# Kernel optimization log

Measured on AMD Instinct MI355X. Metric: run time of the kernel, lower is better.

## Reference

```python
import jax, jax.numpy as jnp
import numpy as np

B, H, S, D = 2, 16, 2048, 64


def setup_inputs() -> dict:
    key = jax.random.key(0)
    kq, kk, kv = jax.random.split(key, 3)
    queries = jax.random.normal(kq, (B, H, S, D), dtype=jnp.float32)
    keys = jax.random.normal(kk, (B, H, S, D), dtype=jnp.float32)
    values = jax.random.normal(kv, (B, H, S, D), dtype=jnp.float32)
    scaling_factor = jnp.asarray(np.sqrt(D), dtype=jnp.float32)
    # causal mask, broadcast over heads: True = attend
    causal = jnp.tril(jnp.ones((S, S), dtype=bool))
    mask = jnp.broadcast_to(causal[None, None, :, :], (B, 1, S, S))
    return {
        "queries": queries,
        "keys": keys,
        "values": values,
        "scaling_factor": scaling_factor,
        "mask": mask,
    }


def reference(queries, keys, values, scaling_factor, mask):
    # scores: [B, H, S, S]
    scores = jnp.einsum("bhqd,bhkd->bhqk", queries, keys) / scaling_factor
    scores = jnp.where(mask, scores, -jnp.inf)
    attn = jax.nn.softmax(scores, axis=-1)
    # embeddings: [B, H, S, D]
    return jnp.einsum("bhqk,bhkd->bhqd", attn, values)
```

## Files before the change

kernel.cpp:

```cpp
#include <hip/hip_runtime.h>
#include <hip/hip_bf16.h>


typedef __attribute__((ext_vector_type(8))) short bf16x8;
typedef __attribute__((ext_vector_type(4))) float f32x4;
typedef unsigned uint2v __attribute__((ext_vector_type(2)));

#define MFMA32K(a, b, c) __builtin_amdgcn_mfma_f32_16x16x32_bf16(a, b, c, 0, 0, 0)

constexpr int Bsz = 2, Hn = 16, Sn = 2048, Dn = 64;
constexpr int KBLK = 64;
constexpr int NE = Bsz * Hn * Sn * Dn;

#if defined(__has_builtin)
#if __has_builtin(__builtin_amdgcn_exp2f)
#define EXP2(x) __builtin_amdgcn_exp2f(x)
#endif
#endif
#ifndef EXP2
#define EXP2(x) exp2f(x)
#endif

__device__ inline short f2bf(float f) {
  union { float f; unsigned u; } v;
  v.f = f;
  unsigned r = v.u + 0x7FFF + ((v.u >> 16) & 1);
  return (short)(r >> 16);
}

__device__ inline unsigned pk_bf16(float lo, float hi) {
  unsigned r;
  asm("v_cvt_pk_bf16_f32 %0, %1, %2" : "=v"(r) : "v"(lo), "v"(hi));
  return r;
}

__device__ inline void gl2lds16(const void* g, void* l) {
  __builtin_amdgcn_global_load_lds(
      (const __attribute__((address_space(1))) unsigned int*)g,
      (__attribute__((address_space(3))) unsigned int*)l, 16, 0, 0);
}

__device__ inline int swz(int row, int colbyte) {
  return row * 128 + (colbyte ^ ((row & 7) << 4));
}

#if defined(__has_builtin)
#if __has_builtin(__builtin_amdgcn_permlane16_swap) && \
    __has_builtin(__builtin_amdgcn_permlane32_swap)
#define HAVE_PERMLANE_SWAP 1
#endif
#endif

__device__ inline float xred_max(float x) {
#ifdef HAVE_PERMLANE_SWAP
  uint2v a = __builtin_amdgcn_permlane16_swap(__float_as_uint(x),
                                              __float_as_uint(x), false, false);
  x = fmaxf(__uint_as_float(a[0]), __uint_as_float(a[1]));
  uint2v b = __builtin_amdgcn_permlane32_swap(__float_as_uint(x),
                                              __float_as_uint(x), false, false);
  x = fmaxf(__uint_as_float(b[0]), __uint_as_float(b[1]));
#else
  x = fmaxf(x, __shfl_xor(x, 16, 64));
  x = fmaxf(x, __shfl_xor(x, 32, 64));
#endif
  return x;
}

__global__ __launch_bounds__(256) void prep(const float* __restrict__ K,
                                            const float* __restrict__ V,
                                            short* __restrict__ Kb,
                                            short* __restrict__ Vt) {
  __shared__ short t[64][66];
  const int tile = blockIdx.x, bh = blockIdx.y;
  const int tid = threadIdx.x;
  const int r = tid >> 2, c = (tid & 3) * 16;
  const size_t base = (size_t)bh * Sn * Dn;

  {
    const float* kp = K + base + (size_t)(tile * 64 + r) * Dn + c;
    float4 x0 = *(const float4*)(kp + 0);
    float4 x1 = *(const float4*)(kp + 4);
    float4 x2 = *(const float4*)(kp + 8);
    float4 x3 = *(const float4*)(kp + 12);
    bf16x8 w0, w1;
    w0[0] = f2bf(x0.x); w0[1] = f2bf(x0.y); w0[2] = f2bf(x0.z); w0[3] = f2bf(x0.w);
    w0[4] = f2bf(x1.x); w0[5] = f2bf(x1.y); w0[6] = f2bf(x1.z); w0[7] = f2bf(x1.w);
    w1[0] = f2bf(x2.x); w1[1] = f2bf(x2.y); w1[2] = f2bf(x2.z); w1[3] = f2bf(x2.w);
    w1[4] = f2bf(x3.x); w1[5] = f2bf(x3.y); w1[6] = f2bf(x3.z); w1[7] = f2bf(x3.w);
    short* op = Kb + base + (size_t)(tile * 64 + r) * Dn + c;
    *(bf16x8*)op = w0;
    *(bf16x8*)(op + 8) = w1;
  }
  {
    const float* vp = V + base + (size_t)(tile * 64 + r) * Dn + c;
    float4 x0 = *(const float4*)(vp + 0);
    float4 x1 = *(const float4*)(vp + 4);
    float4 x2 = *(const float4*)(vp + 8);
    float4 x3 = *(const float4*)(vp + 12);
    short* tr = &t[r][c];
    tr[0] = f2bf(x0.x); tr[1] = f2bf(x0.y); tr[2] = f2bf(x0.z); tr[3] = f2bf(x0.w);
    tr[4] = f2bf(x1.x); tr[5] = f2bf(x1.y); tr[6] = f2bf(x1.z); tr[7] = f2bf(x1.w);
    tr[8] = f2bf(x2.x); tr[9] = f2bf(x2.y); tr[10] = f2bf(x2.z); tr[11] = f2bf(x2.w);
    tr[12] = f2bf(x3.x); tr[13] = f2bf(x3.y); tr[14] = f2bf(x3.z); tr[15] = f2bf(x3.w);
    __syncthreads();
    short* op = Vt + base + (size_t)r * Sn + tile * 64 + c;
    bf16x8 w0, w1;
#pragma unroll
    for (int j = 0; j < 8; ++j) {
      int p0 = c + j, p1 = c + 8 + j;
      int k0 = 32 * (p0 >> 5) + 16 * ((p0 >> 2) & 1) + 4 * ((p0 >> 3) & 3) + (p0 & 3);
      int k1 = 32 * (p1 >> 5) + 16 * ((p1 >> 2) & 1) + 4 * ((p1 >> 3) & 3) + (p1 & 3);
      w0[j] = t[k0][r];
      w1[j] = t[k1][r];
    }
    *(bf16x8*)op = w0;
    *(bf16x8*)(op + 8) = w1;
  }
}

__global__ __launch_bounds__(256, 4) void attn_fwd(
    const float* __restrict__ Q, const short* __restrict__ Kb,
    const short* __restrict__ Vt, const float* __restrict__ SF,
    float* __restrict__ O) {
  __shared__ short Kbuf[2][64 * 64];
  __shared__ short Vbuf[2][64 * 64];

  const int bh = blockIdx.x;
  const int qt = (gridDim.y - 1) - blockIdx.y;
  const int tid = threadIdx.x;
  const int wave = tid >> 6, lane = tid & 63;
  const int qh = wave >> 1, par = wave & 1;
  const int g = lane >> 4, lc = lane & 15;
  const float qscale = 1.4426950408889634f / SF[0];

  const size_t base = (size_t)bh * Sn * Dn;
  const char* Kg = (const char*)(Kb + base);
  const char* Vg = (const char*)(Vt + base);
  const int nkv = qt + 1;
  const int npairs = (nkv + 1) >> 1;

  int qg[2];
  qg[0] = qt * 64 + qh * 32 + lc;
  qg[1] = qg[0] + 16;

  int ka[4][2], va[2][4];
#pragma unroll
  for (int t = 0; t < 4; ++t) {
    ka[t][0] = swz(t * 16 + lc, g * 16);
    ka[t][1] = swz(t * 16 + lc, g * 16 + 64);
  }
#pragma unroll
  for (int t2 = 0; t2 < 2; ++t2)
#pragma unroll
    for (int dt = 0; dt < 4; ++dt)
      va[t2][dt] = swz(dt * 16 + lc, t2 * 64 + g * 16);
  int koff[2], voff[2];
#pragma unroll
  for (int j = 0; j < 2; ++j) {
    int off = (wave * 2 + j) * 1024 + lane * 16;
    int row = off >> 7;
    int col = (off & 127) ^ ((row & 7) << 4);
    koff[j] = row * 128 + col;
    voff[j] = row * 4096 + col;
  }

  auto stageK = [&](int kt, int buf) {
    const char* src = Kg + (size_t)kt * 8192;
#pragma unroll
    for (int j = 0; j < 2; ++j)
      gl2lds16(src + koff[j], (char*)Kbuf[buf] + (wave * 2 + j) * 1024);
  };
  auto stageV = [&](int kt, int buf) {
    const char* src = Vg + (size_t)kt * 128;
#pragma unroll
    for (int j = 0; j < 2; ++j)
      gl2lds16(src + voff[j], (char*)Vbuf[buf] + (wave * 2 + j) * 1024);
  };

  bf16x8 bq[2][2];
#pragma unroll
  for (int u = 0; u < 2; ++u) {
    const float* qp = Q + base + (size_t)qg[u] * Dn + g * 8;
#pragma unroll
    for (int h = 0; h < 2; ++h) {
      float4 x0 = *(const float4*)(qp + 32 * h);
      float4 x1 = *(const float4*)(qp + 32 * h + 4);
      bf16x8 a;
      a[0] = f2bf(x0.x * qscale); a[1] = f2bf(x0.y * qscale);
      a[2] = f2bf(x0.z * qscale); a[3] = f2bf(x0.w * qscale);
      a[4] = f2bf(x1.x * qscale); a[5] = f2bf(x1.y * qscale);
      a[6] = f2bf(x1.z * qscale); a[7] = f2bf(x1.w * qscale);
      bq[u][h] = a;
    }
  }

  bf16x8 ones;
#pragma unroll
  for (int j = 0; j < 8; ++j) ones[j] = (short)0x3F80;

  f32x4 o[2][4], lsum[2];
  float m[2] = {-10000.0f, -10000.0f};
#pragma unroll
  for (int u = 0; u < 2; ++u) {
    lsum[u] = (f32x4){0.f, 0.f, 0.f, 0.f};
#pragma unroll
    for (int dt = 0; dt < 4; ++dt) o[u][dt] = (f32x4){0.f, 0.f, 0.f, 0.f};
  }

  stageK(0, 0);
  stageV(0, 0);
  if (nkv > 1) { stageK(1, 1); stageV(1, 1); }
  __syncthreads();

  for (int j = 0; j < npairs; ++j) {
    const int myt = 2 * j + par;
    if (myt < nkv) {
      const char* Kc = (const char*)Kbuf[par];
      const char* Vc = (const char*)Vbuf[par];

      f32x4 s[2][4];
      __builtin_amdgcn_s_setprio(1);
#pragma unroll
      for (int t = 0; t < 4; ++t) {
        bf16x8 ak0 = *(const bf16x8*)(Kc + ka[t][0]);
        bf16x8 ak1 = *(const bf16x8*)(Kc + ka[t][1]);
#pragma unroll
        for (int u = 0; u < 2; ++u) {
          f32x4 z = (f32x4){0.f, 0.f, 0.f, 0.f};
          z = MFMA32K(ak0, bq[u][0], z);
          z = MFMA32K(ak1, bq[u][1], z);
          s[u][t] = z;
        }
      }
      __builtin_amdgcn_s_setprio(0);

      if (myt == qt) {
        const int kb = myt * KBLK;
#pragma unroll
        for (int u = 0; u < 2; ++u)
#pragma unroll
          for (int t = 0; t < 4; ++t)
#pragma unroll
            for (int i = 0; i < 4; ++i) {
              int kg = kb + t * 16 + g * 4 + i;
              if (kg > qg[u]) s[u][t][i] = -30000.0f;
            }
      }

      union { unsigned uu[4]; bf16x8 v; } pb[2][2];
#pragma unroll
      for (int u = 0; u < 2; ++u) {
        float a0 = fmaxf(fmaxf(s[u][0][0], s[u][0][1]), s[u][0][2]);
        float a1 = fmaxf(fmaxf(s[u][0][3], s[u][1][0]), s[u][1][1]);
        float a2 = fmaxf(fmaxf(s[u][1][2], s[u][1][3]), s[u][2][0]);
        float a3 = fmaxf(fmaxf(s[u][2][1], s[u][2][2]), s[u][2][3]);
        float a4 = fmaxf(fmaxf(s[u][3][0], s[u][3][1]), s[u][3][2]);
        float b0 = fmaxf(fmaxf(a0, a1), a2);
        float b1 = fmaxf(fmaxf(a3, a4), s[u][3][3]);
        float plocal = fmaxf(b0, b1);
        if (!__all(plocal - m[u] <= 8.0f)) {
          float pmax = xred_max(plocal);
          float mnew = fmaxf(m[u], pmax);
          float alpha = EXP2(m[u] - mnew);
          lsum[u][0] *= alpha;
#pragma unroll
          for (int dt = 0; dt < 4; ++dt) o[u][dt] *= alpha;
          m[u] = mnew;
        }
#pragma unroll
        for (int t = 0; t < 4; ++t)
#pragma unroll
          for (int i = 0; i < 4; ++i) s[u][t][i] = EXP2(s[u][t][i] - m[u]);
#pragma unroll
        for (int t2 = 0; t2 < 2; ++t2) {
          pb[u][t2].uu[0] = pk_bf16(s[u][2 * t2][0], s[u][2 * t2][1]);
          pb[u][t2].uu[1] = pk_bf16(s[u][2 * t2][2], s[u][2 * t2][3]);
          pb[u][t2].uu[2] = pk_bf16(s[u][2 * t2 + 1][0], s[u][2 * t2 + 1][1]);
          pb[u][t2].uu[3] = pk_bf16(s[u][2 * t2 + 1][2], s[u][2 * t2 + 1][3]);
        }
      }

      __builtin_amdgcn_s_setprio(1);
#pragma unroll
      for (int t2 = 0; t2 < 2; ++t2) {
        lsum[0] = MFMA32K(ones, pb[0][t2].v, lsum[0]);
        lsum[1] = MFMA32K(ones, pb[1][t2].v, lsum[1]);
#pragma unroll
        for (int dt = 0; dt < 4; ++dt) {
          bf16x8 av = *(const bf16x8*)(Vc + va[t2][dt]);
          o[0][dt] = MFMA32K(av, pb[0][t2].v, o[0][dt]);
          o[1][dt] = MFMA32K(av, pb[1][t2].v, o[1][dt]);
        }
      }
      __builtin_amdgcn_s_setprio(0);
    }

    __syncthreads();

    const int nt0 = 2 * j + 2;
    if (nt0 < nkv) { stageK(nt0, 0); stageV(nt0, 0); }
    if (nt0 + 1 < nkv) { stageK(nt0 + 1, 1); stageV(nt0 + 1, 1); }
    __syncthreads();
  }

  float* scr = (qh == 0) ? (float*)&Kbuf[0][0] : (float*)&Vbuf[0][0];
  if (par == 1) {
#pragma unroll
    for (int u = 0; u < 2; ++u) {
#pragma unroll
      for (int dt = 0; dt < 4; ++dt)
        *(f32x4*)(scr + (u * 16 + lc) * 64 + dt * 16 + g * 4) = o[u][dt];
      if (g == 0) {
        scr[2048 + u * 16 + lc] = m[u];
        scr[2080 + u * 16 + lc] = lsum[u][0];
      }
    }
  }
  __syncthreads();
  if (par == 0) {
#pragma unroll
    for (int u = 0; u < 2; ++u) {
      float mB = scr[2048 + u * 16 + lc];
      float lB = scr[2080 + u * 16 + lc];
      float M = fmaxf(m[u], mB);
      float aA = EXP2(m[u] - M), aB = EXP2(mB - M);
      float inv = 1.0f / (lsum[u][0] * aA + lB * aB);
      float cA = aA * inv, cB = aB * inv;
      float* op = O + base + (size_t)qg[u] * Dn;
#pragma unroll
      for (int dt = 0; dt < 4; ++dt) {
        f32x4 oB = *(const f32x4*)(scr + (u * 16 + lc) * 64 + dt * 16 + g * 4);
        f32x4 r = o[u][dt] * cA + oB * cB;
        *(f32x4*)(op + dt * 16 + g * 4) = r;
      }
    }
  }
}

extern "C" void kernel_launch(void* const* d_in, const int* in_sizes, int n_in,
                              void* d_out, int out_size, void* d_ws, size_t ws_size,
                              hipStream_t stream) {
  const float* Q = (const float*)d_in[0];
  const float* K = (const float*)d_in[1];
  const float* V = (const float*)d_in[2];
  const float* SF = (const float*)d_in[3];
  float* O = (float*)d_out;

  short* Kb = (short*)d_ws;
  short* Vt = Kb + NE;

  prep<<<dim3(Sn / 64, Bsz * Hn), 256, 0, stream>>>(K, V, Kb, Vt);
  attn_fwd<<<dim3(Bsz * Hn, Sn / 64), 256, 0, stream>>>(Q, Kb, Vt, SF, O);
}
```

Before: 44.39 us.

## Split long causal query tiles across two KV chunks with a combine kernel

Query tiles 16-31, the ones with the longest causal KV ranges, are now each split into two blocks covering KV tiles 0-15 and 16-qt. Each block writes an unnormalized partial output plus its max and sum to workspace, and a new combine kernel merges them with log-sum-exp rescaling. The aim is to shorten the critical path of the heaviest blocks and balance the load across the grid (48 y-blocks instead of 32). In exchange it adds an extra kernel launch, partial-output traffic through global memory, and extra workspace that must fit in the provided buffer.

```diff
diff --git a/kernel.cpp b/kernel.cpp
--- a/kernel.cpp
+++ b/kernel.cpp
@@ -11,6 +11,7 @@
 constexpr int Bsz = 2, Hn = 16, Sn = 2048, Dn = 64;
 constexpr int KBLK = 64;
 constexpr int NE = Bsz * Hn * Sn * Dn;
+constexpr int NPART = Bsz * Hn * 16 * 2;
 
 #if defined(__has_builtin)
 #if __has_builtin(__builtin_amdgcn_exp2f)
@@ -121,12 +122,18 @@
 __global__ __launch_bounds__(256, 4) void attn_fwd(
     const float* __restrict__ Q, const short* __restrict__ Kb,
     const short* __restrict__ Vt, const float* __restrict__ SF,
-    float* __restrict__ O) {
+    float* __restrict__ O, float* __restrict__ Opart,
+    float* __restrict__ MLpart) {
   __shared__ short Kbuf[2][64 * 64];
   __shared__ short Vbuf[2][64 * 64];
 
   const int bh = blockIdx.x;
-  const int qt = (gridDim.y - 1) - blockIdx.y;
+  const int qy = blockIdx.y;
+  const int qt = (qy < 16) ? (31 - qy) : (47 - qy);
+  const int chunk = (qy >= 16 && qy < 32) ? 1 : 0;
+  const int t0 = chunk * 16;
+  const int t1 = (qy < 16) ? 15 : qt;
+
   const int tid = threadIdx.x;
   const int wave = tid >> 6, lane = tid & 63;
   const int qh = wave >> 1, par = wave & 1;
@@ -136,8 +143,6 @@
   const size_t base = (size_t)bh * Sn * Dn;
   const char* Kg = (const char*)(Kb + base);
   const char* Vg = (const char*)(Vt + base);
-  const int nkv = qt + 1;
-  const int npairs = (nkv + 1) >> 1;
 
   int qg[2];
   qg[0] = qt * 64 + qh * 32 + lc;
@@ -207,14 +212,15 @@
     for (int dt = 0; dt < 4; ++dt) o[u][dt] = (f32x4){0.f, 0.f, 0.f, 0.f};
   }
 
-  stageK(0, 0);
-  stageV(0, 0);
-  if (nkv > 1) { stageK(1, 1); stageV(1, 1); }
+  stageK(t0, 0);
+  stageV(t0, 0);
+  if (t0 + 1 <= t1) { stageK(t0 + 1, 1); stageV(t0 + 1, 1); }
   __syncthreads();
 
+  const int npairs = ((t1 - t0 + 1) + 1) >> 1;
   for (int j = 0; j < npairs; ++j) {
-    const int myt = 2 * j + par;
-    if (myt < nkv) {
+    const int myt = t0 + 2 * j + par;
+    if (myt <= t1) {
       const char* Kc = (const char*)Kbuf[par];
       const char* Vc = (const char*)Vbuf[par];
 
@@ -297,9 +303,9 @@
 
     __syncthreads();
 
-    const int nt0 = 2 * j + 2;
-    if (nt0 < nkv) { stageK(nt0, 0); stageV(nt0, 0); }
-    if (nt0 + 1 < nkv) { stageK(nt0 + 1, 1); stageV(nt0 + 1, 1); }
+    const int nt0 = t0 + 2 * j + 2;
+    if (nt0 <= t1) { stageK(nt0, 0); stageV(nt0, 0); }
+    if (nt0 + 1 <= t1) { stageK(nt0 + 1, 1); stageV(nt0 + 1, 1); }
     __syncthreads();
   }
 
@@ -324,16 +330,61 @@
       float lB = scr[2080 + u * 16 + lc];
       float M = fmaxf(m[u], mB);
       float aA = EXP2(m[u] - M), aB = EXP2(mB - M);
-      float inv = 1.0f / (lsum[u][0] * aA + lB * aB);
-      float cA = aA * inv, cB = aB * inv;
-      float* op = O + base + (size_t)qg[u] * Dn;
-#pragma unroll
-      for (int dt = 0; dt < 4; ++dt) {
-        f32x4 oB = *(const f32x4*)(scr + (u * 16 + lc) * 64 + dt * 16 + g * 4);
-        f32x4 r = o[u][dt] * cA + oB * cB;
-        *(f32x4*)(op + dt * 16 + g * 4) = r;
+      float lC = lsum[u][0] * aA + lB * aB;
+      if (qy >= 32) {
+        float inv = 1.0f / lC;
+        float cA = aA * inv, cB = aB * inv;
+        float* op = O + base + (size_t)qg[u] * Dn;
+#pragma unroll
+        for (int dt = 0; dt < 4; ++dt) {
+          f32x4 oB = *(const f32x4*)(scr + (u * 16 + lc) * 64 + dt * 16 + g * 4);
+          f32x4 r = o[u][dt] * cA + oB * cB;
+          *(f32x4*)(op + dt * 16 + g * 4) = r;
+        }
+      } else {
+        const int p = (bh * 16 + (qt - 16)) * 2 + chunk;
+        const int row = qh * 32 + u * 16 + lc;
+        float* op = Opart + (size_t)p * 4096 + row * 64;
+#pragma unroll
+        for (int dt = 0; dt < 4; ++dt) {
+          f32x4 oB = *(const f32x4*)(scr + (u * 16 + lc) * 64 + dt * 16 + g * 4);
+          f32x4 r = o[u][dt] * aA + oB * aB;
+          *(f32x4*)(op + dt * 16 + g * 4) = r;
+        }
+        if (g == 0) ((float2*)MLpart)[p * 64 + row] = make_float2(M, lC);
       }
     }
+  }
+}
+
+__global__ __launch_bounds__(256) void combine(const float* __restrict__ Opart,
+                                               const float* __restrict__ MLpart,
+                                               float* __restrict__ O) {
+  const int bx = blockIdx.x;
+  const int bh = bx >> 4, qh = bx & 15, qt = 16 + qh;
+  const int p0 = (bh * 16 + qh) * 2;
+  const int tid = threadIdx.x;
+  const int r = tid >> 2, dc = (tid & 3) * 16;
+
+  const float2 ml0 = ((const float2*)MLpart)[p0 * 64 + r];
+  const float2 ml1 = ((const float2*)MLpart)[(p0 + 1) * 64 + r];
+  const float M = fmaxf(ml0.x, ml1.x);
+  const float s0 = EXP2(ml0.x - M), s1 = EXP2(ml1.x - M);
+  const float inv = 1.0f / (ml0.y * s0 + ml1.y * s1);
+
+  const float* a = Opart + (size_t)p0 * 4096 + r * 64 + dc;
+  const float* b = a + 4096;
+  float* op = O + (size_t)bh * Sn * Dn + (size_t)(qt * 64 + r) * Dn + dc;
+#pragma unroll
+  for (int j = 0; j < 4; ++j) {
+    float4 x = *(const float4*)(a + j * 4);
+    float4 y = *(const float4*)(b + j * 4);
+    float4 z;
+    z.x = (x.x * s0 + y.x * s1) * inv;
+    z.y = (x.y * s0 + y.y * s1) * inv;
+    z.z = (x.z * s0 + y.z * s1) * inv;
+    z.w = (x.w * s0 + y.w * s1) * inv;
+    *(float4*)(op + j * 4) = z;
   }
 }
 
@@ -348,7 +399,11 @@
 
   short* Kb = (short*)d_ws;
   short* Vt = Kb + NE;
+  float* Opart = (float*)(Vt + NE);
+  float* MLpart = Opart + (size_t)NPART * 4096;
 
   prep<<<dim3(Sn / 64, Bsz * Hn), 256, 0, stream>>>(K, V, Kb, Vt);
-  attn_fwd<<<dim3(Bsz * Hn, Sn / 64), 256, 0, stream>>>(Q, Kb, Vt, SF, O);
-}
+  attn_fwd<<<dim3(Bsz * Hn, 48), 256, 0, stream>>>(Q, Kb, Vt, SF, O, Opart,
+                                                   MLpart);
+  combine<<<dim3(Bsz * Hn * 16), 256, 0, stream>>>(Opart, MLpart, O);
+}
```

Measured after the change: 54.25 us. 22.2% more time.
